# Kernel optimization log

Hardware: AMD Instinct MI355X
Metric: run time of the kernel (lower is better)

## Reference

```python
import jax, jax.numpy as jnp
import numpy as np

N_NODES = 100000
N_EDGES = 1000000
N_GRAPHS = 512
IN_DIM = 3
HID = 64


def setup_inputs() -> dict:
    key = jax.random.key(0)
    ks = jax.random.split(key, 7)
    x = jax.random.normal(ks[0], (N_NODES, IN_DIM), dtype=jnp.float32)
    edge_index = jax.random.randint(ks[1], (2, N_EDGES), 0, N_NODES, dtype=jnp.int64)
    batch = jnp.sort(jax.random.randint(ks[2], (N_NODES,), 0, N_GRAPHS, dtype=jnp.int64))
    # Glorot-ish init for GCNConv linear weights (PyG uses glorot), zero bias.
    W1 = jax.random.normal(ks[3], (IN_DIM, HID), dtype=jnp.float32) / np.float32(np.sqrt(IN_DIM))
    b1 = jnp.zeros((HID,), dtype=jnp.float32)
    W2 = jax.random.normal(ks[4], (HID, HID), dtype=jnp.float32) / np.float32(np.sqrt(HID))
    b2 = jnp.zeros((HID,), dtype=jnp.float32)
    return {"x": x, "W1": W1, "b1": b1, "W2": W2, "b2": b2,
            "edge_index": edge_index, "batch": batch}


def reference(x, W1, b1, W2, b2, edge_index, batch):
    n = x.shape[0]
    loop = jnp.arange(n)
    # GCNConv adds self-loops, then symmetric normalization D^-1/2 (A+I) D^-1/2
    src = jnp.concatenate([edge_index[0], loop])  # [E+N]
    dst = jnp.concatenate([edge_index[1], loop])  # [E+N]
    deg = jax.ops.segment_sum(jnp.ones(dst.shape[0], x.dtype), dst, num_segments=n)
    dinv = jnp.where(deg > 0, jax.lax.rsqrt(deg), 0.0)
    norm = dinv[src] * dinv[dst]  # [E+N]

    def gcn_conv(h, W, b):
        hw = h @ W                       # [N, out] linear first (PyG order)
        msg = hw[src] * norm[:, None]    # gather + scale, [E+N, out]
        agg = jax.ops.segment_sum(msg, dst, num_segments=n)  # scatter-add
        return agg + b

    h = jax.nn.relu(gcn_conv(x, W1, b1))
    h = jax.nn.relu(gcn_conv(h, W2, b2))

    # global_mean_pool over the batch vector
    sums = jax.ops.segment_sum(h, batch, num_segments=N_GRAPHS)          # [G, HID]
    counts = jax.ops.segment_sum(jnp.ones(n, h.dtype), batch, num_segments=N_GRAPHS)
    return sums / jnp.maximum(counts, 1.0)[:, None]
```

## Files before the change

### kernel.cpp

```cpp
#include <hip/hip_runtime.h>

#define HID 64
#define N_GRAPHS_C 512
#define BSHIFT 8
#define NBUCK_MAX 512
#define CAP 3264
#define EPB 4096

typedef unsigned short u16;
typedef unsigned int u32;
typedef unsigned long long u64;

__device__ __forceinline__ float bf2f(u16 u) {
    union { u32 i; float f; } v; v.i = ((u32)u) << 16; return v.f;
}
__device__ __forceinline__ u16 f2bf(float f) {
    union { float f; u32 i; } v; v.f = f;
    u32 x = v.i;
    return (u16)((x + 0x7fffu + ((x >> 16) & 1u)) >> 16);
}


__global__ void bin_pairs(const int* __restrict__ src, const int* __restrict__ dst,
                          int* __restrict__ gcursor, u32* __restrict__ pairs,
                          int nE, int nbuck) {
    __shared__ int lh[NBUCK_MAX];
    __shared__ int lbase[NBUCK_MAX];
    int t = threadIdx.x;
    lh[t] = 0; lh[t + 256] = 0;
    __syncthreads();
    int base = blockIdx.x * EPB;
    u32 pk[16]; int rj[16], bj[16];
    #pragma unroll
    for (int j = 0; j < 16; ++j) {
        int e = base + j * 256 + t;
        if (e < nE) {
            int s = src[e], d = dst[e];
            bj[j] = d >> BSHIFT;
            pk[j] = ((u32)(d & 255) << 17) | (u32)s;
            rj[j] = atomicAdd(&lh[bj[j]], 1);
        } else {
            bj[j] = -1;
        }
    }
    __syncthreads();
    for (int b = t; b < nbuck; b += 256)
        lbase[b] = (lh[b] > 0) ? atomicAdd(&gcursor[b], lh[b]) : 0;
    __syncthreads();
    #pragma unroll
    for (int j = 0; j < 16; ++j) {
        if (bj[j] >= 0) {
            int pos = bj[j] * CAP + lbase[bj[j]] + rj[j];
            pairs[pos] = pk[j];
        }
    }
}

__global__ void build_csr(const u32* __restrict__ pairs, const int* __restrict__ gcursor,
                          int* __restrict__ csr_src, int2* __restrict__ off2,
                          float* __restrict__ dinv, const float* __restrict__ x,
                          float4* __restrict__ xs, u16* __restrict__ A16, int n) {
    __shared__ int hist[256];
    __shared__ int tmp[256];
    int t = threadIdx.x;
    int b = blockIdx.x;
    int pbeg = b * CAP;
    int pend = pbeg + gcursor[b];
    hist[t] = 0;
    if (b == 0 && t < 32) ((u32*)(A16 + (size_t)n * HID))[t] = 0;
    __syncthreads();
    for (int i = pbeg + t; i < pend; i += 256)
        atomicAdd(&hist[pairs[i] >> 17], 1);
    __syncthreads();
    int v = hist[t];
    tmp[t] = v;
    __syncthreads();
    for (int d = 1; d < 256; d <<= 1) {
        int add = (t >= d) ? tmp[t - d] : 0;
        __syncthreads();
        tmp[t] += add;
        __syncthreads();
    }
    int e = pbeg + tmp[t] - v;
    int node = (b << BSHIFT) + t;
    if (node < n) {
        float dv = rsqrtf((float)(v + 1));
        off2[node] = make_int2(e, e + v);
        dinv[node] = dv;
        xs[node] = make_float4(x[3*node]*dv, x[3*node+1]*dv, x[3*node+2]*dv, dv);
    }
    hist[t] = e;
    __syncthreads();
    for (int i = pbeg + t; i < pend; i += 256) {
        u32 p = pairs[i];
        int pos = atomicAdd(&hist[p >> 17], 1);
        csr_src[pos] = (int)(p & 0x1FFFFu);
    }
}


__global__ void agg3(const float4* __restrict__ xs, const int* __restrict__ csr_src,
                     const int2* __restrict__ off2, float4* __restrict__ agg4, int n) {
    int node = blockIdx.x * blockDim.x + threadIdx.x;
    if (node >= n) return;
    int2 be = off2[node];
    int beg = be.x, end = be.y;
    float4 self = xs[node];
    float a0 = 0.f, a1 = 0.f, a2 = 0.f;
    for (int k = beg; k < end; k += 8) {
        int e1 = end - 1;
        int idx[8];
        float4 v[8];
        #pragma unroll
        for (int j = 0; j < 8; ++j) idx[j] = csr_src[min(k + j, e1)];
        #pragma unroll
        for (int j = 0; j < 8; ++j) v[j] = xs[idx[j]];
        #pragma unroll
        for (int j = 0; j < 8; ++j) {
            if (k + j < end) { a0 += v[j].x; a1 += v[j].y; a2 += v[j].z; }
        }
    }
    agg4[node] = make_float4(a0 + self.x, a1 + self.y, a2 + self.z, self.w);
}


#define MM2_NODES 32
__global__ void mm2f(const float4* __restrict__ agg4, const float* __restrict__ W1,
                     const float* __restrict__ b1, const float* __restrict__ W2,
                     u16* __restrict__ A16, int n) {
    __shared__ float w[HID * HID];
    __shared__ float h[MM2_NODES * HID];
    __shared__ float dd[MM2_NODES];
    int t = threadIdx.x;
    for (int i = t; i < HID * HID; i += 256) w[i] = W2[i];
    int base = blockIdx.x * MM2_NODES;
    for (int i = t; i < MM2_NODES * HID; i += 256) {
        int node = base + (i >> 6);
        int f = i & 63;
        float hv = 0.0f;
        if (node < n) {
            float4 a = agg4[node];
            float v = (a.x * W1[f] + a.y * W1[HID + f] + a.z * W1[2 * HID + f]) * a.w + b1[f];
            hv = v > 0.0f ? v : 0.0f;
            if (f == 0) dd[i >> 6] = a.w;
        }
        h[i] = hv;
    }
    __syncthreads();
    int f = t & 63, g = t >> 6;
    float acc[8];
    #pragma unroll
    for (int j = 0; j < 8; ++j) acc[j] = 0.0f;
    #pragma unroll 4
    for (int k = 0; k < HID; ++k) {
        float wk = w[k * HID + f];
        #pragma unroll
        for (int j = 0; j < 8; ++j) acc[j] += h[(g * 8 + j) * HID + k] * wk;
    }
    #pragma unroll
    for (int j = 0; j < 8; ++j) {
        int node = base + g * 8 + j;
        if (node < n) A16[(size_t)node * HID + f] = f2bf(acc[j] * dd[g * 8 + j]);
    }
}


__global__ void gather_nodes(const u16* __restrict__ A16, const float* __restrict__ dinv,
                             const int* __restrict__ csr_src, const int2* __restrict__ off2,
                             const float* __restrict__ bias,
                             u16* __restrict__ H16, int n) {
    int t = threadIdx.x;
    int waveq = t >> 4;
    int m = t & 15;
    int qbase = t & 48;
    int node = blockIdx.x * 16 + waveq;
    if (node >= n) return;
    int2 be = off2[node];
    int beg = be.x, end = be.y;
    u64 selfrow = *(const u64*)(A16 + ((size_t)node << 6) + (m << 2));
    u32 slo = (u32)selfrow, shi = (u32)(selfrow >> 32);
    float acc0 = bf2f((u16)(slo & 0xffffu));
    float acc1 = bf2f((u16)(slo >> 16));
    float acc2 = bf2f((u16)(shi & 0xffffu));
    float acc3 = bf2f((u16)(shi >> 16));
    const char* Ab = (const char*)A16;
    u32 laneoff = (u32)(m << 3);
    for (int k = beg; k < end; k += 16) {
        int nIdx = end - k;
        int myIdx = (m < nIdx) ? csr_src[k + m] : n;
        #pragma unroll
        for (int j0 = 0; j0 < 16; j0 += 8) {
            int ss[8]; u64 rows[8];
            #pragma unroll
            for (int j = 0; j < 8; ++j)
                ss[j] = __shfl(myIdx, qbase + j0 + j, 64);
            #pragma unroll
            for (int j = 0; j < 8; ++j)
                rows[j] = *(const u64*)(Ab + (((u32)ss[j] << 7) | laneoff));
            #pragma unroll
            for (int j = 0; j < 8; ++j) {
                u32 lo = (u32)rows[j], hi = (u32)(rows[j] >> 32);
                acc0 += bf2f((u16)(lo & 0xffffu));
                acc1 += bf2f((u16)(lo >> 16));
                acc2 += bf2f((u16)(hi & 0xffffu));
                acc3 += bf2f((u16)(hi >> 16));
            }
        }
    }
    float ddv = dinv[node];
    float4 bb = *(const float4*)(bias + (m << 2));
    float v0 = fmaxf(acc0 * ddv + bb.x, 0.0f);
    float v1 = fmaxf(acc1 * ddv + bb.y, 0.0f);
    float v2 = fmaxf(acc2 * ddv + bb.z, 0.0f);
    float v3 = fmaxf(acc3 * ddv + bb.w, 0.0f);
    u64 outp = (u64)f2bf(v0) | ((u64)f2bf(v1) << 16)
             | ((u64)f2bf(v2) << 32) | ((u64)f2bf(v3) << 48);
    *(u64*)(H16 + ((size_t)node << 6) + (m << 2)) = outp;
}


__device__ __forceinline__ int lower_bound(const int* __restrict__ a, int n, int key) {
    int lo = 0, hi = n;
    while (lo < hi) {
        int mid = (lo + hi) >> 1;
        if (a[mid] < key) lo = mid + 1; else hi = mid;
    }
    return lo;
}

__global__ void pool_graph(const u16* __restrict__ H16, const int* __restrict__ batch,
                           float* __restrict__ out, int n) {
    int g = blockIdx.x;
    int t = threadIdx.x;
    int lo = lower_bound(batch, n, g);
    int hi = lower_bound(batch, n, g + 1);
    int cntN = hi - lo;
    int sid = t >> 4;
    int m = t & 15;
    float a0 = 0.f, a1 = 0.f, a2 = 0.f, a3 = 0.f;
    int i = lo + sid;
    for (; i + 16 < hi; i += 32) {
        u64 r0 = *(const u64*)(H16 + ((size_t)i << 6) + (m << 2));
        u64 r1 = *(const u64*)(H16 + ((size_t)(i + 16) << 6) + (m << 2));
        u32 l0 = (u32)r0, h0 = (u32)(r0 >> 32);
        u32 l1 = (u32)r1, h1 = (u32)(r1 >> 32);
        a0 += bf2f((u16)(l0 & 0xffffu)) + bf2f((u16)(l1 & 0xffffu));
        a1 += bf2f((u16)(l0 >> 16))     + bf2f((u16)(l1 >> 16));
        a2 += bf2f((u16)(h0 & 0xffffu)) + bf2f((u16)(h1 & 0xffffu));
        a3 += bf2f((u16)(h0 >> 16))     + bf2f((u16)(h1 >> 16));
    }
    if (i < hi) {
        u64 r0 = *(const u64*)(H16 + ((size_t)i << 6) + (m << 2));
        u32 l0 = (u32)r0, h0 = (u32)(r0 >> 32);
        a0 += bf2f((u16)(l0 & 0xffffu));
        a1 += bf2f((u16)(l0 >> 16));
        a2 += bf2f((u16)(h0 & 0xffffu));
        a3 += bf2f((u16)(h0 >> 16));
    }
    a0 += __shfl_xor(a0, 16, 64); a0 += __shfl_xor(a0, 32, 64);
    a1 += __shfl_xor(a1, 16, 64); a1 += __shfl_xor(a1, 32, 64);
    a2 += __shfl_xor(a2, 16, 64); a2 += __shfl_xor(a2, 32, 64);
    a3 += __shfl_xor(a3, 16, 64); a3 += __shfl_xor(a3, 32, 64);
    __shared__ float smf[4 * HID];
    int wave = t >> 6, lane = t & 63;
    if (lane < 16) {
        smf[wave * HID + 4 * lane + 0] = a0;
        smf[wave * HID + 4 * lane + 1] = a1;
        smf[wave * HID + 4 * lane + 2] = a2;
        smf[wave * HID + 4 * lane + 3] = a3;
    }
    __syncthreads();
    if (t < HID) {
        float s = smf[t] + smf[HID + t] + smf[2 * HID + t] + smf[3 * HID + t];
        out[(size_t)g * HID + t] = s / fmaxf((float)cntN, 1.0f);
    }
}


extern "C" void kernel_launch(void* const* d_in, const int* in_sizes, int n_in,
                              void* d_out, int out_size, void* d_ws, size_t ws_size,
                              hipStream_t stream) {
    const float* x  = (const float*)d_in[0];
    const float* W1 = (const float*)d_in[1];
    const float* b1 = (const float*)d_in[2];
    const float* W2 = (const float*)d_in[3];
    const float* b2 = (const float*)d_in[4];
    const int*   ei = (const int*)d_in[5];
    const int*   batch = (const int*)d_in[6];

    const int n  = in_sizes[0] / 3;
    const int nE = in_sizes[5] / 2;
    const int* src = ei;
    const int* dst = ei + nE;
    const int nbuck = (n + ((1 << BSHIFT) - 1)) >> BSHIFT;
    const int nGraphs = out_size / HID;

    char* p = (char*)d_ws;
    int*    gcursor = (int*)p;                p += 2048;
    int*    csr_src = (int*)p;                p += (size_t)nbuck * CAP * 4;
    int2*   off2    = (int2*)p;               p += (size_t)n * 8;
    float*  dinv    = (float*)p;              p += (size_t)n * 4;
    float4* xs      = (float4*)p;             p += (size_t)n * 16;
    float4* agg4    = (float4*)p;             p += (size_t)n * 16;
    u16*    A16     = (u16*)p;                p += (size_t)(n + 1) * HID * 2;
    u16*    H2      = (u16*)p;                p += (size_t)n * HID * 2;
    u32*    pairs   = (u32*)A16;

    const int BT = 256;
    const int gridNode = (n + BT - 1) / BT;
    const int gridE2   = (nE + EPB - 1) / EPB;
    const int gridMM2  = (n + MM2_NODES - 1) / MM2_NODES;
    const int gridGath = (n + 15) / 16;

    hipMemsetAsync(gcursor, 0, 2048, stream);
    bin_pairs<<<gridE2, BT, 0, stream>>>(src, dst, gcursor, pairs, nE, nbuck);
    build_csr<<<nbuck, BT, 0, stream>>>(pairs, gcursor, csr_src, off2, dinv, x, xs, A16, n);

    agg3<<<gridNode, BT, 0, stream>>>(xs, csr_src, off2, agg4, n);
    mm2f<<<gridMM2, BT, 0, stream>>>(agg4, W1, b1, W2, A16, n);

    gather_nodes<<<gridGath, BT, 0, stream>>>(A16, dinv, csr_src, off2, b2, H2, n);

    pool_graph<<<nGraphs, BT, 0, stream>>>(H2, batch, (float*)d_out, n);
}
```

Baseline: 169.0 us.

## Drop CSR build and aggregate directly from bucketed pairs with LDS atomics

Removes the CSR construction (prefix scan and scatter into csr_src/offsets) and instead aggregates both GCN layers straight from the destination-bucketed edge pairs. Each block owns one 256-node bucket and accumulates messages in shared memory with float atomics, then adds the self term, normalization, bias and ReLU. This saves a pass over the edges and the CSR writes, but relies on heavy LDS atomic traffic. Layer 2 also needs a 64KB shared accumulator per block, which lowers occupancy, and the gathers become per-feature 2-byte loads. Float atomic ordering makes the summation order nondeterministic.

```diff
diff --git a/kernel.cpp b/kernel.cpp
--- a/kernel.cpp
+++ b/kernel.cpp
@@ -56,71 +56,64 @@
     }
 }
 
-__global__ void build_csr(const u32* __restrict__ pairs, const int* __restrict__ gcursor,
-                          int* __restrict__ csr_src, int2* __restrict__ off2,
-                          float* __restrict__ dinv, const float* __restrict__ x,
-                          float4* __restrict__ xs, u16* __restrict__ A16, int n) {
+
+__global__ void node_prep(const u32* __restrict__ pairs, const int* __restrict__ gcursor,
+                          const float* __restrict__ x, float* __restrict__ dinv,
+                          float4* __restrict__ xs, int n) {
     __shared__ int hist[256];
-    __shared__ int tmp[256];
     int t = threadIdx.x;
     int b = blockIdx.x;
-    int pbeg = b * CAP;
-    int pend = pbeg + gcursor[b];
     hist[t] = 0;
-    if (b == 0 && t < 32) ((u32*)(A16 + (size_t)n * HID))[t] = 0;
-    __syncthreads();
-    for (int i = pbeg + t; i < pend; i += 256)
-        atomicAdd(&hist[pairs[i] >> 17], 1);
-    __syncthreads();
-    int v = hist[t];
-    tmp[t] = v;
-    __syncthreads();
-    for (int d = 1; d < 256; d <<= 1) {
-        int add = (t >= d) ? tmp[t - d] : 0;
-        __syncthreads();
-        tmp[t] += add;
-        __syncthreads();
-    }
-    int e = pbeg + tmp[t] - v;
+    __syncthreads();
+    int pbeg = b * CAP, cnt = gcursor[b];
+    for (int i = t; i < cnt; i += 256)
+        atomicAdd(&hist[pairs[pbeg + i] >> 17], 1);
+    __syncthreads();
     int node = (b << BSHIFT) + t;
     if (node < n) {
-        float dv = rsqrtf((float)(v + 1));
-        off2[node] = make_int2(e, e + v);
+        float dv = rsqrtf((float)(hist[t] + 1));
         dinv[node] = dv;
         xs[node] = make_float4(x[3*node]*dv, x[3*node+1]*dv, x[3*node+2]*dv, dv);
     }
-    hist[t] = e;
-    __syncthreads();
-    for (int i = pbeg + t; i < pend; i += 256) {
-        u32 p = pairs[i];
-        int pos = atomicAdd(&hist[p >> 17], 1);
-        csr_src[pos] = (int)(p & 0x1FFFFu);
-    }
-}
-
-
-__global__ void agg3(const float4* __restrict__ xs, const int* __restrict__ csr_src,
-                     const int2* __restrict__ off2, float4* __restrict__ agg4, int n) {
-    int node = blockIdx.x * blockDim.x + threadIdx.x;
-    if (node >= n) return;
-    int2 be = off2[node];
-    int beg = be.x, end = be.y;
-    float4 self = xs[node];
-    float a0 = 0.f, a1 = 0.f, a2 = 0.f;
-    for (int k = beg; k < end; k += 8) {
-        int e1 = end - 1;
-        int idx[8];
-        float4 v[8];
-        #pragma unroll
-        for (int j = 0; j < 8; ++j) idx[j] = csr_src[min(k + j, e1)];
-        #pragma unroll
-        for (int j = 0; j < 8; ++j) v[j] = xs[idx[j]];
-        #pragma unroll
-        for (int j = 0; j < 8; ++j) {
-            if (k + j < end) { a0 += v[j].x; a1 += v[j].y; a2 += v[j].z; }
-        }
-    }
-    agg4[node] = make_float4(a0 + self.x, a1 + self.y, a2 + self.z, self.w);
+}
+
+
+__global__ void agg_l1(const u32* __restrict__ pairs, const int* __restrict__ gcursor,
+                       const float4* __restrict__ xs, float4* __restrict__ agg4, int n) {
+    __shared__ float a0[256], a1[256], a2[256];
+    int t = threadIdx.x;
+    int b = blockIdx.x;
+    a0[t] = 0.0f; a1[t] = 0.0f; a2[t] = 0.0f;
+    __syncthreads();
+    int pbeg = b * CAP, cnt = gcursor[b];
+    int k = t;
+    for (; k + 768 < cnt; k += 1024) {
+        u32 p0 = pairs[pbeg + k];
+        u32 p1 = pairs[pbeg + k + 256];
+        u32 p2 = pairs[pbeg + k + 512];
+        u32 p3 = pairs[pbeg + k + 768];
+        float4 v0 = xs[p0 & 0x1FFFFu];
+        float4 v1 = xs[p1 & 0x1FFFFu];
+        float4 v2 = xs[p2 & 0x1FFFFu];
+        float4 v3 = xs[p3 & 0x1FFFFu];
+        int d0 = p0 >> 17, d1 = p1 >> 17, d2 = p2 >> 17, d3 = p3 >> 17;
+        atomicAdd(&a0[d0], v0.x); atomicAdd(&a1[d0], v0.y); atomicAdd(&a2[d0], v0.z);
+        atomicAdd(&a0[d1], v1.x); atomicAdd(&a1[d1], v1.y); atomicAdd(&a2[d1], v1.z);
+        atomicAdd(&a0[d2], v2.x); atomicAdd(&a1[d2], v2.y); atomicAdd(&a2[d2], v2.z);
+        atomicAdd(&a0[d3], v3.x); atomicAdd(&a1[d3], v3.y); atomicAdd(&a2[d3], v3.z);
+    }
+    for (; k < cnt; k += 256) {
+        u32 p = pairs[pbeg + k];
+        float4 v = xs[p & 0x1FFFFu];
+        int d = p >> 17;
+        atomicAdd(&a0[d], v.x); atomicAdd(&a1[d], v.y); atomicAdd(&a2[d], v.z);
+    }
+    __syncthreads();
+    int node = (b << BSHIFT) + t;
+    if (node < n) {
+        float4 self = xs[node];
+        agg4[node] = make_float4(a0[t] + self.x, a1[t] + self.y, a2[t] + self.z, self.w);
+    }
 }
 
 
@@ -165,57 +158,50 @@
 }
 
 
-__global__ void gather_nodes(const u16* __restrict__ A16, const float* __restrict__ dinv,
-                             const int* __restrict__ csr_src, const int2* __restrict__ off2,
-                             const float* __restrict__ bias,
-                             u16* __restrict__ H16, int n) {
-    int t = threadIdx.x;
-    int waveq = t >> 4;
-    int m = t & 15;
-    int qbase = t & 48;
-    int node = blockIdx.x * 16 + waveq;
-    if (node >= n) return;
-    int2 be = off2[node];
-    int beg = be.x, end = be.y;
-    u64 selfrow = *(const u64*)(A16 + ((size_t)node << 6) + (m << 2));
-    u32 slo = (u32)selfrow, shi = (u32)(selfrow >> 32);
-    float acc0 = bf2f((u16)(slo & 0xffffu));
-    float acc1 = bf2f((u16)(slo >> 16));
-    float acc2 = bf2f((u16)(shi & 0xffffu));
-    float acc3 = bf2f((u16)(shi >> 16));
-    const char* Ab = (const char*)A16;
-    u32 laneoff = (u32)(m << 3);
-    for (int k = beg; k < end; k += 16) {
-        int nIdx = end - k;
-        int myIdx = (m < nIdx) ? csr_src[k + m] : n;
-        #pragma unroll
-        for (int j0 = 0; j0 < 16; j0 += 8) {
-            int ss[8]; u64 rows[8];
-            #pragma unroll
-            for (int j = 0; j < 8; ++j)
-                ss[j] = __shfl(myIdx, qbase + j0 + j, 64);
-            #pragma unroll
-            for (int j = 0; j < 8; ++j)
-                rows[j] = *(const u64*)(Ab + (((u32)ss[j] << 7) | laneoff));
-            #pragma unroll
-            for (int j = 0; j < 8; ++j) {
-                u32 lo = (u32)rows[j], hi = (u32)(rows[j] >> 32);
-                acc0 += bf2f((u16)(lo & 0xffffu));
-                acc1 += bf2f((u16)(lo >> 16));
-                acc2 += bf2f((u16)(hi & 0xffffu));
-                acc3 += bf2f((u16)(hi >> 16));
-            }
+#define L2BT 512
+__global__ void agg_l2(const u32* __restrict__ pairs, const int* __restrict__ gcursor,
+                       const u16* __restrict__ A16, const float* __restrict__ dinv,
+                       const float* __restrict__ bias, u16* __restrict__ H2, int n) {
+    __shared__ float acc[256 * HID];
+    int t = threadIdx.x;
+    int b = blockIdx.x;
+    for (int i = t; i < 256 * HID; i += L2BT) acc[i] = 0.0f;
+    __syncthreads();
+    int pbeg = b * CAP, cnt = gcursor[b];
+    int w = t >> 6;
+    int f = t & 63;
+    const int NW = L2BT / 64;
+    int k = w;
+    for (; k + 3 * NW < cnt; k += 4 * NW) {
+        u32 p0 = pairs[pbeg + k];
+        u32 p1 = pairs[pbeg + k + NW];
+        u32 p2 = pairs[pbeg + k + 2 * NW];
+        u32 p3 = pairs[pbeg + k + 3 * NW];
+        u16 r0 = A16[((size_t)(p0 & 0x1FFFFu) << 6) + f];
+        u16 r1 = A16[((size_t)(p1 & 0x1FFFFu) << 6) + f];
+        u16 r2 = A16[((size_t)(p2 & 0x1FFFFu) << 6) + f];
+        u16 r3 = A16[((size_t)(p3 & 0x1FFFFu) << 6) + f];
+        atomicAdd(&acc[((p0 >> 17) << 6) + f], bf2f(r0));
+        atomicAdd(&acc[((p1 >> 17) << 6) + f], bf2f(r1));
+        atomicAdd(&acc[((p2 >> 17) << 6) + f], bf2f(r2));
+        atomicAdd(&acc[((p3 >> 17) << 6) + f], bf2f(r3));
+    }
+    for (; k < cnt; k += NW) {
+        u32 p = pairs[pbeg + k];
+        u16 r = A16[((size_t)(p & 0x1FFFFu) << 6) + f];
+        atomicAdd(&acc[((p >> 17) << 6) + f], bf2f(r));
+    }
+    __syncthreads();
+    int nbeg = b << BSHIFT;
+    for (int i = t; i < 256 * HID; i += L2BT) {
+        int node = nbeg + (i >> 6);
+        if (node < n) {
+            int ff = i & 63;
+            float self = bf2f(A16[((size_t)node << 6) + ff]);
+            float v = (acc[i] + self) * dinv[node] + bias[ff];
+            H2[((size_t)node << 6) + ff] = f2bf(fmaxf(v, 0.0f));
         }
     }
-    float ddv = dinv[node];
-    float4 bb = *(const float4*)(bias + (m << 2));
-    float v0 = fmaxf(acc0 * ddv + bb.x, 0.0f);
-    float v1 = fmaxf(acc1 * ddv + bb.y, 0.0f);
-    float v2 = fmaxf(acc2 * ddv + bb.z, 0.0f);
-    float v3 = fmaxf(acc3 * ddv + bb.w, 0.0f);
-    u64 outp = (u64)f2bf(v0) | ((u64)f2bf(v1) << 16)
-             | ((u64)f2bf(v2) << 32) | ((u64)f2bf(v3) << 48);
-    *(u64*)(H16 + ((size_t)node << 6) + (m << 2)) = outp;
 }
 
 
@@ -297,29 +283,25 @@
 
     char* p = (char*)d_ws;
     int*    gcursor = (int*)p;                p += 2048;
-    int*    csr_src = (int*)p;                p += (size_t)nbuck * CAP * 4;
-    int2*   off2    = (int2*)p;               p += (size_t)n * 8;
+    u32*    pairs   = (u32*)p;                p += (size_t)nbuck * CAP * 4;
     float*  dinv    = (float*)p;              p += (size_t)n * 4;
     float4* xs      = (float4*)p;             p += (size_t)n * 16;
     float4* agg4    = (float4*)p;             p += (size_t)n * 16;
-    u16*    A16     = (u16*)p;                p += (size_t)(n + 1) * HID * 2;
+    u16*    A16     = (u16*)p;                p += (size_t)n * HID * 2;
     u16*    H2      = (u16*)p;                p += (size_t)n * HID * 2;
-    u32*    pairs   = (u32*)A16;
 
     const int BT = 256;
-    const int gridNode = (n + BT - 1) / BT;
     const int gridE2   = (nE + EPB - 1) / EPB;
     const int gridMM2  = (n + MM2_NODES - 1) / MM2_NODES;
-    const int gridGath = (n + 15) / 16;
 
     hipMemsetAsync(gcursor, 0, 2048, stream);
     bin_pairs<<<gridE2, BT, 0, stream>>>(src, dst, gcursor, pairs, nE, nbuck);
-    build_csr<<<nbuck, BT, 0, stream>>>(pairs, gcursor, csr_src, off2, dinv, x, xs, A16, n);
-
-    agg3<<<gridNode, BT, 0, stream>>>(xs, csr_src, off2, agg4, n);
+    node_prep<<<nbuck, BT, 0, stream>>>(pairs, gcursor, x, dinv, xs, n);
+
+    agg_l1<<<nbuck, BT, 0, stream>>>(pairs, gcursor, xs, agg4, n);
     mm2f<<<gridMM2, BT, 0, stream>>>(agg4, W1, b1, W2, A16, n);
 
-    gather_nodes<<<gridGath, BT, 0, stream>>>(A16, dinv, csr_src, off2, b2, H2, n);
+    agg_l2<<<nbuck, L2BT, 0, stream>>>(pairs, gcursor, A16, dinv, b2, H2, n);
 
     pool_graph<<<nGraphs, BT, 0, stream>>>(H2, batch, (float*)d_out, n);
 }
```

New measurement: 595.8 us. +252.6%, slower.
